# Performance work log

Measured on AMD Instinct MI355X. Metric: run time of the kernel, lower is better.

## Reference

```python
import jax, jax.numpy as jnp
import numpy as np

D = 1024; DI = 2048; HS = 16; PS = DI // HS; NS = 64; KC = 4; CHUNK = 64
HA = 16; HKV = 4; PA = D // HA; MLP_MULT = 4; ROPE_BASE = 10000.0
B_SZ = 2; L_SEQ = 2048


def rms_norm(x):
    eps = jnp.asarray(jnp.finfo(x.dtype).eps, x.dtype)
    return x * jax.lax.rsqrt(jnp.mean(jnp.square(x), axis=-1, keepdims=True) + eps)


def silu(x):
    return x * jax.nn.sigmoid(x)


def apply_rope(x, cos, sin):
    half = x.shape[-1] // 2
    x1, x2 = x[..., :half], x[..., half:]
    return jnp.concatenate([x1 * cos + x2 * sin, -x1 * sin + x2 * cos], axis=-1)


def selective_scan(x, A, Bm, Cm, dt, chunk):
    # x: [B,L,H,P], Bm/Cm: [B,L,H,N], A/dt: [H]. L must be a multiple of chunk.
    Bb, L, H, P = x.shape
    N = Bm.shape[-1]
    decay = jnp.exp(A * dt)  # [H]
    nc = L // chunk
    xp = x.reshape(Bb, nc, chunk, H, P).transpose(0, 1, 3, 2, 4)   # [B,nc,H,cs,P]
    Bp = Bm.reshape(Bb, nc, chunk, H, N).transpose(0, 1, 3, 2, 4)  # [B,nc,H,cs,N]
    Cp = Cm.reshape(Bb, nc, chunk, H, N).transpose(0, 1, 3, 2, 4)
    x_dt = xp * dt[None, None, :, None, None]
    idx = jnp.arange(chunk)
    diff = idx[:, None] - idx[None, :]
    # intra-chunk causal decay matrix L_mat: [H,cs,cs]
    Lm = jnp.where(diff >= 0, decay[:, None, None] ** jnp.maximum(diff, 0), 0.0)
    CB = jnp.einsum('bchqn,bchkn->bchqk', Cp, Bp)
    y_diag = jnp.einsum('bchqk,bchkp->bchqp', CB * Lm[None, None], x_dt)
    # per-chunk states
    decay_rev = decay[:, None] ** (chunk - 1 - idx)[None, :]  # [H,cs]
    states = jnp.einsum('bchtn,bchtp->bchnp', Bp * decay_rev[None, None, :, :, None], x_dt)
    # inter-chunk propagation
    ci = jnp.arange(nc)
    shift = ci[:, None] - ci[None, :] - 1
    cdec = decay ** chunk
    M = jnp.where(shift >= 0, cdec[:, None, None] ** jnp.maximum(shift, 0), 0.0)  # [H,nc,nc]
    h_carry = jnp.einsum('hij,bjhnp->bihnp', M, states)
    decay_out = decay[:, None] ** (idx + 1)[None, :]  # [H,cs]
    y_off = jnp.einsum('bchtn,bchnp->bchtp', Cp, h_carry) * decay_out[None, None, :, :, None]
    y = (y_diag + y_off).transpose(0, 1, 3, 2, 4).reshape(Bb, L, H, P)
    return y


def mlp(n, fc_w, proj_w):
    h = jax.nn.relu(n @ fc_w)
    return jnp.square(h) @ proj_w


def setup_inputs() -> dict:
    key = jax.random.key(0)
    ks = jax.random.split(key, 24)
    w = lambda k, shp, s=0.02: jax.random.normal(k, shp, jnp.float32) * s
    dt_init = jax.random.uniform(ks[0], (HS,), jnp.float32, 0.001, 0.1)
    dt_bias = dt_init + jnp.log(-jnp.expm1(-dt_init))  # inverse softplus
    return {
        'x': jax.random.normal(ks[1], (B_SZ, L_SEQ, D), jnp.float32),
        'in_proj_w': w(ks[2], (D, 2 * DI)),
        'conv_w': w(ks[3], (DI, KC), 0.2),
        'conv_b': jnp.zeros((DI,), jnp.float32),
        'B_proj_w': w(ks[4], (D, HS * NS)),
        'C_proj_w': w(ks[5], (D, HS * NS)),
        'dt_bias': dt_bias,
        'A_log': jnp.log(jnp.arange(1, HS + 1, dtype=jnp.float32)),
        'D_param': jnp.ones((HS,), jnp.float32),
        'out_proj_w': w(ks[6], (DI, D)),
        'resid_mix_m': jnp.stack([jnp.ones(D), jnp.zeros(D)]).astype(jnp.float32),
        'mamba_scale': jnp.ones((D,), jnp.float32),
        'm_fc_w': w(ks[7], (D, MLP_MULT * D)),
        'm_proj_w': w(ks[8], (MLP_MULT * D, D)),
        'm_mlp_scale': jnp.ones((D,), jnp.float32),
        'resid_mix_a': jnp.stack([jnp.ones(D), jnp.zeros(D)]).astype(jnp.float32),
        'q_w': w(ks[9], (D, D)),
        'k_w': w(ks[10], (D, HKV * PA)),
        'v_w': w(ks[11], (D, HKV * PA)),
        'o_w': w(ks[12], (D, D)),
        'q_gain': jnp.full((HA,), 1.0, jnp.float32),
        'attn_scale': jnp.ones((D,), jnp.float32),
        'a_fc_w': w(ks[13], (D, MLP_MULT * D)),
        'a_proj_w': w(ks[14], (MLP_MULT * D, D)),
        'a_mlp_scale': jnp.ones((D,), jnp.float32),
    }


def reference(x, in_proj_w, conv_w, conv_b, B_proj_w, C_proj_w, dt_bias, A_log, D_param, out_proj_w, resid_mix_m, mamba_scale, m_fc_w, m_proj_w, m_mlp_scale, resid_mix_a, q_w, k_w, v_w, o_w, q_gain, attn_scale, a_fc_w, a_proj_w, a_mlp_scale):
    Bb, L, _ = x.shape
    x0 = x
    # ---- Mamba block ----
    xm = resid_mix_m[0][None, None] * x + resid_mix_m[1][None, None] * x0
    n = rms_norm(xm)
    vg = n @ in_proj_w
    value, gate = vg[..., :DI], vg[..., DI:]
    v_t = value.transpose(0, 2, 1)  # [B, DI, L]
    v_conv = jax.lax.conv_general_dilated(
        v_t, conv_w[:, None, :], (1,), [(KC - 1, 0)],
        feature_group_count=DI, dimension_numbers=('NCH', 'OIH', 'NCH')) + conv_b[None, :, None]
    value = silu(v_conv).transpose(0, 2, 1).reshape(Bb, L, HS, PS)
    Bm = (xm @ B_proj_w).reshape(Bb, L, HS, NS)  # B/C use pre-norm (mixed) input
    Cm = (xm @ C_proj_w).reshape(Bb, L, HS, NS)
    dt = jax.nn.softplus(dt_bias)
    A = -jnp.exp(A_log)
    y = selective_scan(value, A, Bm, Cm, dt, CHUNK)
    y = y + D_param[None, None, :, None] * value
    y = (y.reshape(Bb, L, DI) * silu(gate)) @ out_proj_w
    xm = xm + mamba_scale[None, None] * y
    xm = xm + m_mlp_scale[None, None] * mlp(rms_norm(xm), m_fc_w, m_proj_w)
    # ---- Attention block ----
    xa = resid_mix_a[0][None, None] * xm + resid_mix_a[1][None, None] * x0
    n = rms_norm(xa)
    q = (n @ q_w).reshape(Bb, L, HA, PA).transpose(0, 2, 1, 3)
    k = (n @ k_w).reshape(Bb, L, HKV, PA).transpose(0, 2, 1, 3)
    v = (n @ v_w).reshape(Bb, L, HKV, PA).transpose(0, 2, 1, 3)
    q = rms_norm(q); k = rms_norm(k)
    inv_freq = 1.0 / (ROPE_BASE ** (jnp.arange(0, PA, 2, dtype=jnp.float32) / PA))
    f = jnp.outer(jnp.arange(L, dtype=jnp.float32), inv_freq)
    cos, sin = jnp.cos(f)[None, None], jnp.sin(f)[None, None]
    q = apply_rope(q, cos, sin) * q_gain[None, :, None, None]
    k = apply_rope(k, cos, sin)
    G = HA // HKV
    k = jnp.repeat(k, G, axis=1); v = jnp.repeat(v, G, axis=1)
    s = jnp.einsum('bhqd,bhkd->bhqk', q, k) / np.float32(np.sqrt(PA))
    mask = jnp.tril(jnp.ones((L, L), bool))
    s = jnp.where(mask[None, None], s, jnp.asarray(-jnp.inf, s.dtype))
    att = jax.nn.softmax(s, axis=-1)
    y = jnp.einsum('bhqk,bhkd->bhqd', att, v).transpose(0, 2, 1, 3).reshape(Bb, L, D)
    xa = xa + attn_scale[None, None] * (y @ o_w)
    xa = xa + a_mlp_scale[None, None] * mlp(rms_norm(xa), a_fc_w, a_proj_w)
    return xa
```

## Files before the change

kernel.cpp:

```cpp
#include <hip/hip_runtime.h>
#include <hip/hip_bf16.h>
#include <math.h>

#define D_ 1024
#define DI_ 2048
#define HS_ 16
#define PS_ 128
#define NS_ 64
#define HA_ 16
#define HKV_ 4
#define PA_ 64
#define B_ 2
#define L_ 2048
#define NT_ 4096
#define NC_ 32
#define RMS_EPS_ 1.1920929e-7f

typedef __attribute__((ext_vector_type(8))) short short8;
typedef __attribute__((ext_vector_type(4))) float f32x4;

#define GLOAD_LDS16(gp, lp)                                                        \
  __builtin_amdgcn_global_load_lds(                                               \
      (const __attribute__((address_space(1))) unsigned int*)(gp),                \
      (__attribute__((address_space(3))) unsigned int*)(lp), 16, 0, 0)

__global__ __launch_bounds__(256) void transpose_cvt(
    const float* __restrict__ W, __hip_bfloat16* __restrict__ Wt, int K, int N, int ldw) {
  __shared__ float t[32][33];
  int n0 = blockIdx.x * 32, k0 = blockIdx.y * 32;
  int tx = threadIdx.x & 31, ty = threadIdx.x >> 5;
#pragma unroll
  for (int i = 0; i < 4; i++)
    t[ty + i * 8][tx] = W[(size_t)(k0 + ty + i * 8) * ldw + n0 + tx];
  __syncthreads();
#pragma unroll
  for (int i = 0; i < 4; i++)
    Wt[(size_t)(n0 + ty + i * 8) * K + k0 + tx] = __float2bfloat16(t[tx][ty + i * 8]);
}

template<int MODE>
__global__ __launch_bounds__(512) void gemm256_k32(
    const unsigned short* __restrict__ A, const unsigned short* __restrict__ Wt,
    __hip_bfloat16* __restrict__ Cb, int N, int K) {
  __shared__ unsigned short As[3][256 * 32];
  __shared__ unsigned short Bs[3][256 * 32];
  int lid = blockIdx.x;
  int x = lid & 7, r = lid >> 3;
  int bm = ((x >> 2) * 8 + (r & 7)) * 256;
  int bn = ((x & 3) * 4 + (r >> 3)) * 256;
  int tid = threadIdx.x;
  int w = tid >> 6, l = tid & 63;
  int wr = w >> 2, wc = w & 3;
  int l15 = l & 15, lg = l >> 4;
  int rr = tid >> 2, ss = tid & 3;

  f32x4 acc[8][4];
#pragma unroll
  for (int i = 0; i < 8; i++)
#pragma unroll
    for (int j = 0; j < 4; j++) acc[i][j] = (f32x4){0.f, 0.f, 0.f, 0.f};

  auto STAGE = [&](int kt, int nb) {
    int k0 = kt * 32;
#pragma unroll
    for (int p = 0; p < 2; p++) {
      int row = p * 128 + rr;
      int kq = ss ^ ((row >> 1) & 3);
      GLOAD_LDS16(A + (size_t)(bm + row) * K + k0 + kq * 8, &As[nb][row * 32 + ss * 8]);
    }
#pragma unroll
    for (int p = 0; p < 2; p++) {
      int row = p * 128 + rr;
      int kq = ss ^ ((row >> 1) & 3);
      GLOAD_LDS16(Wt + (size_t)(bn + row) * K + k0 + kq * 8, &Bs[nb][row * 32 + ss * 8]);
    }
  };

  int KT = K >> 5;
  STAGE(0, 0);
  STAGE(1, 1);
  int buf = 0;
  for (int t = 0; t < KT; ++t) {
    if (t + 1 < KT) {
      asm volatile("s_waitcnt vmcnt(4)" ::: "memory");
    } else {
      asm volatile("s_waitcnt vmcnt(0)" ::: "memory");
    }
    __builtin_amdgcn_s_barrier();
    __builtin_amdgcn_sched_barrier(0);
    if (t + 2 < KT) STAGE(t + 2, (t + 2) % 3);
    short8 bf[4];
#pragma unroll
    for (int j = 0; j < 4; j++) {
      int row = wc * 64 + j * 16 + l15;
      bf[j] = *(const short8*)&Bs[buf][row * 32 + ((lg ^ ((row >> 1) & 3)) << 3)];
    }
#pragma unroll
    for (int i = 0; i < 8; i++) {
      int row = wr * 128 + i * 16 + l15;
      short8 af = *(const short8*)&As[buf][row * 32 + ((lg ^ ((row >> 1) & 3)) << 3)];
#pragma unroll
      for (int j = 0; j < 4; j++)
        acc[i][j] = __builtin_amdgcn_mfma_f32_16x16x32_bf16(af, bf[j], acc[i][j], 0, 0, 0);
    }
    buf = (buf == 2) ? 0 : buf + 1;
  }
#pragma unroll
  for (int i = 0; i < 8; i++)
#pragma unroll
    for (int j = 0; j < 4; j++) {
      int gr = bm + wr * 128 + i * 16 + lg * 4;
      int gc = bn + wc * 64 + j * 16 + l15;
#pragma unroll
      for (int reg = 0; reg < 4; reg++) {
        float v = acc[i][j][reg];
        if (MODE == 1) { v = fmaxf(v, 0.f); v = v * v; }
        Cb[(size_t)(gr + reg) * N + gc] = __float2bfloat16(v);
      }
    }
}
// ... 23 lines not shown
  int tid = threadIdx.x;
  int w = tid >> 6, l = tid & 63;
  int wr = w / nWc, wc = w % nWc;
  int l15 = l & 15, lg = l >> 4;
  f32x4 acc[MF][4];
#pragma unroll
  for (int i = 0; i < MF; i++)
#pragma unroll
    for (int j = 0; j < 4; j++) acc[i][j] = (f32x4){0.f, 0.f, 0.f, 0.f};
  int r_ = tid >> 3;
  int s_ = tid & 7;

  auto STAGE = [&](int k0, int nb) {
#pragma unroll
    for (int i = 0; i < 4; i++) {
      int rr = i * 32 + r_;
      int kq = s_ ^ (rr & 7);
      GLOAD_LDS16(A + (size_t)(bm + rr) * K + k0 + kq * 8, &As[nb][rr * 64 + s_ * 8]);
    }
#pragma unroll
    for (int i = 0; i < BN / 32; i++) {
      int rr = i * 32 + r_;
      int kq = s_ ^ (rr & 7);
      GLOAD_LDS16(Wt + (size_t)(bn + rr) * K + k0 + kq * 8, &Bs[nb][rr * 64 + s_ * 8]);
    }
  };

  STAGE(0, 0);
  __syncthreads();
  int cur = 0;
  for (int k0 = 0; k0 < K; k0 += 64) {
    if (k0 + 64 < K) STAGE(k0 + 64, cur ^ 1);
#pragma unroll
    for (int h = 0; h < 2; h++) {
      short8 af[MF], bfr[4];
#pragma unroll
      for (int i = 0; i < MF; i++) {
        int row = wr * (16 * MF) + i * 16 + l15;
        int c = h * 4 + lg;
        af[i] = *(const short8*)&As[cur][row * 64 + ((c ^ (row & 7)) << 3)];
      }
#pragma unroll
      for (int j = 0; j < 4; j++) {
        int row = wc * 64 + j * 16 + l15;
        int c = h * 4 + lg;
        bfr[j] = *(const short8*)&Bs[cur][row * 64 + ((c ^ (row & 7)) << 3)];
      }
#pragma unroll
      for (int i = 0; i < MF; i++)
#pragma unroll
        for (int j = 0; j < 4; j++)
          acc[i][j] = __builtin_amdgcn_mfma_f32_16x16x32_bf16(af[i], bfr[j], acc[i][j], 0, 0, 0);
    }
    __syncthreads();
    cur ^= 1;
  }
  int rb = lg * 4, cb2 = l15;
#pragma unroll
  for (int i = 0; i < MF; i++)
#pragma unroll
    for (int j = 0; j < 4; j++) {
      int gr = bm + wr * (16 * MF) + i * 16 + rb;
      int gc = bn + wc * 64 + j * 16 + cb2;
#pragma unroll
      for (int reg = 0; reg < 4; reg++) {
        float v = acc[i][j][reg];
        size_t idx = (size_t)(gr + reg) * N + gc;
        if (mode == 0) {
          Cf[idx] = v;
        } else if (mode == 1) {
          v = fmaxf(v, 0.f);
          Cb[idx] = __float2bfloat16(v * v);
        } else if (mode == 2) {
          Cb[idx] = __float2bfloat16(v);
        } else {
          Cf[idx] = baseb[idx] + scale[gc] * v;
        }
      }
    }
}

__global__ __launch_bounds__(256) void gemm64(
    const unsigned short* __restrict__ A, const unsigned short* __restrict__ Wt,
    float* __restrict__ Cf, const float* __restrict__ baseb,
    const float* __restrict__ scale, int N, int K, int mode) {
  __shared__ unsigned short As[2][64 * 64];
  __shared__ unsigned short Bs[2][64 * 64];
  int lid = blockIdx.x;
  int x = lid & 7, r = lid >> 3;
  int bm = (x * 8 + (r & 7)) * 64;
  int bn = (r >> 3) * 64;
  int tid = threadIdx.x;
  int w = tid >> 6, l = tid & 63;
  int l15 = l & 15, lg = l >> 4;
  f32x4 acc[4];
#pragma unroll
  for (int j = 0; j < 4; j++) acc[j] = (f32x4){0.f, 0.f, 0.f, 0.f};
  int r_ = tid >> 3;
  int s_ = tid & 7;

  auto STAGE = [&](int k0, int nb) {
#pragma unroll
    for (int i = 0; i < 2; i++) {
      int row = i * 32 + r_;
      int kq = s_ ^ (row & 7);
      GLOAD_LDS16(A + (size_t)(bm + row) * K + k0 + kq * 8, &As[nb][row * 64 + s_ * 8]);
    }
#pragma unroll
    for (int i = 0; i < 2; i++) {
      int row = i * 32 + r_;
      int kq = s_ ^ (row & 7);
      GLOAD_LDS16(Wt + (size_t)(bn + row) * K + k0 + kq * 8, &Bs[nb][row * 64 + s_ * 8]);
    }
  };

  STAGE(0, 0);
  __syncthreads();
  int cur = 0;
  for (int k0 = 0; k0 < K; k0 += 64) {
    if (k0 + 64 < K) STAGE(k0 + 64, cur ^ 1);
#pragma unroll
    for (int h = 0; h < 2; h++) {
      int c = h * 4 + lg;
      int arow = w * 16 + l15;
      short8 af = *(const short8*)&As[cur][arow * 64 + ((c ^ (arow & 7)) << 3)];
#pragma unroll
      for (int j = 0; j < 4; j++) {
        int brow = j * 16 + l15;
        short8 bfr = *(const short8*)&Bs[cur][brow * 64 + ((c ^ (brow & 7)) << 3)];
        acc[j] = __builtin_amdgcn_mfma_f32_16x16x32_bf16(af, bfr, acc[j], 0, 0, 0);
      }
    }
    __syncthreads();
    cur ^= 1;
  }
#pragma unroll
  for (int j = 0; j < 4; j++) {
    int gr = bm + w * 16 + lg * 4;
    int gc = bn + j * 16 + l15;
#pragma unroll
    for (int reg = 0; reg < 4; reg++) {
      float v = acc[j][reg];
      size_t idx = (size_t)(gr + reg) * N + gc;
      if (mode == 0) Cf[idx] = v;
      else           Cf[idx] = baseb[idx] + scale[gc] * v;
    }
  }
}

__global__ __launch_bounds__(256) void mix_rms_kernel(
    const float* __restrict__ a, const float* __restrict__ b2,
    const float* __restrict__ mix, float* __restrict__ xout,
    __hip_bfloat16* __restrict__ nbf, __hip_bfloat16* __restrict__ rawbf) {
  int row = blockIdx.x;
  size_t base = (size_t)row * D_;
  float v[4]; float ss = 0.f;
#pragma unroll
  for (int i = 0; i < 4; i++) {
    int d = threadIdx.x + i * 256;
    float val = mix[d] * a[base + d] + mix[D_ + d] * b2[base + d];
    v[i] = val; ss += val * val;
  }
  for (int o = 32; o > 0; o >>= 1) ss += __shfl_down(ss, o, 64);
  __shared__ float red[4];
  if ((threadIdx.x & 63) == 0) red[threadIdx.x >> 6] = ss;
  __syncthreads();
  float inv = rsqrtf((red[0] + red[1] + red[2] + red[3]) * (1.f / D_) + RMS_EPS_);
#pragma unroll
  for (int i = 0; i < 4; i++) {
    int d = threadIdx.x + i * 256;
    xout[base + d] = v[i];
    nbf[base + d] = __float2bfloat16(v[i] * inv);
    if (rawbf) rawbf[base + d] = __float2bfloat16(v[i]);
  }
}

__global__ __launch_bounds__(256) void rms_kernel(
    const float* __restrict__ a, __hip_bfloat16* __restrict__ nbf) {
  int row = blockIdx.x;
  size_t base = (size_t)row * D_;
  float v[4]; float ss = 0.f;
#pragma unroll
  for (int i = 0; i < 4; i++) {
    int d = threadIdx.x + i * 256;
    float val = a[base + d];
    v[i] = val; ss += val * val;
  }
  for (int o = 32; o > 0; o >>= 1) ss += __shfl_down(ss, o, 64);
  __shared__ float red[4];
  if ((threadIdx.x & 63) == 0) red[threadIdx.x >> 6] = ss;
  __syncthreads();
  float inv = rsqrtf((red[0] + red[1] + red[2] + red[3]) * (1.f / D_) + RMS_EPS_);
#pragma unroll
  for (int i = 0; i < 4; i++) {
    int d = threadIdx.x + i * 256;
    nbf[base + d] = __float2bfloat16(v[i] * inv);
  }
}

__global__ __launch_bounds__(256) void conv_silu_kernel(
    const __hip_bfloat16* __restrict__ vg, const float* __restrict__ cw,
    const float* __restrict__ cb, float* __restrict__ xv) {
  int idx = blockIdx.x * 256 + threadIdx.x;
  int c = idx & (DI_ - 1);
  int bl = idx >> 11;
  int l = bl & (L_ - 1);
  float acc = cb[c];
  float w0 = cw[c * 4 + 0], w1 = cw[c * 4 + 1], w2 = cw[c * 4 + 2], w3 = cw[c * 4 + 3];
  size_t rb = (size_t)bl * 4096 + c;
  if (l >= 3) acc += __bfloat162float(vg[rb - (size_t)3 * 4096]) * w0;
  if (l >= 2) acc += __bfloat162float(vg[rb - (size_t)2 * 4096]) * w1;
  if (l >= 1) acc += __bfloat162float(vg[rb - (size_t)1 * 4096]) * w2;
  acc += __bfloat162float(vg[rb]) * w3;
  xv[idx] = acc / (1.f + __expf(-acc));
}

__global__ __launch_bounds__(256) void scanA1_kernel(
    const float* __restrict__ xv, const __hip_bfloat16* __restrict__ BCm,
    const float* __restrict__ dt_bias, const float* __restrict__ A_log,
    float* __restrict__ st) {
  __shared__ __align__(16) float sm[4096 + 8192];
  float* Bs = sm;
  float* Xs = sm + 4096;
  int blk = blockIdx.x;
  int c = blk & 31, h = (blk >> 5) & 15, b = blk >> 9;
  float dt = log1pf(__expf(dt_bias[h]));
  float adt = -__expf(A_log[h]) * dt;
  int tid = threadIdx.x;
  int l0 = c * 64;
  size_t rB = ((size_t)(b * L_ + l0)) * 2048 + h * NS_;
#pragma unroll
  for (int i = 0; i < 16; i++) {
    int e = tid + i * 256;
    int t = e >> 6, n = e & 63;
    Bs[t * 64 + n] = __bfloat162float(BCm[rB + (size_t)t * 2048 + n]);
  }
  size_t rX = ((size_t)(b * L_ + l0)) * DI_ + h * PS_;
#pragma unroll
  for (int i = 0; i < 32; i++) {
    int e = tid + i * 256;
    int t = e >> 7, p = e & 127;
    Xs[t * 128 + p] = xv[rX + (size_t)t * DI_ + p];
  }
  __syncthreads();
  int pg = tid & 31;
  int ng = (tid >> 5) << 3;
  float acc[8][4];
#pragma unroll
  for (int nn = 0; nn < 8; nn++)
#pragma unroll
    for (int i = 0; i < 4; i++) acc[nn][i] = 0.f;
  for (int t = 0; t < 64; t++) {
    float dr = __expf(adt * (float)(63 - t));
    float4 x4 = *(const float4*)&Xs[t * 128 + pg * 4];
    float xd0 = x4.x * dr, xd1 = x4.y * dr, xd2 = x4.z * dr, xd3 = x4.w * dr;
#pragma unroll
    for (int nn = 0; nn < 8; nn++) {
      float bv = Bs[t * 64 + ng + nn];
      acc[nn][0] += bv * xd0; acc[nn][1] += bv * xd1;
      acc[nn][2] += bv * xd2; acc[nn][3] += bv * xd3;
    }
  }
  size_t sb = ((size_t)((b * HS_ + h) * NC_ + c)) * (NS_ * PS_);
#pragma unroll
  for (int nn = 0; nn < 8; nn++) {
    *(float4*)&st[sb + (size_t)(ng + nn) * PS_ + pg * 4] =
        make_float4(acc[nn][0] * dt, acc[nn][1] * dt, acc[nn][2] * dt, acc[nn][3] * dt);
  }
}

__global__ __launch_bounds__(256) void scanA2_kernel(
    const float* __restrict__ xv, const __hip_bfloat16* __restrict__ BCm,
    const float* __restrict__ dt_bias,
    const float* __restrict__ A_log, const float* __restrict__ D_param,
    float* __restrict__ y) {
  __shared__ __align__(16) float sm[4160 + 8192];
  float* Cb = sm;
  float* Bs = sm + 4160;
  float* Xs = sm + 4160;
  int blk = blockIdx.x;
  int c = blk & 31, h = (blk >> 5) & 15, b = blk >> 9;
  float dt = log1pf(__expf(dt_bias[h]));
  float adt = -__expf(A_log[h]) * dt;
  float Dp = D_param[h];
  int tid = threadIdx.x;
  int l0 = c * 64;
  size_t rB = ((size_t)(b * L_ + l0)) * 2048 + h * NS_;
#pragma unroll
  for (int i = 0; i < 16; i++) {
    int e = tid + i * 256;
    int t = e >> 6, n = e & 63;
    Bs[t * 64 + n] = __bfloat162float(BCm[rB + (size_t)t * 2048 + n]);
    Cb[t * 65 + n] = __bfloat162float(BCm[rB + 1024 + (size_t)t * 2048 + n]);
  }
  __syncthreads();
  int q = tid >> 2;
  int kb = (tid & 3) << 4;
  float cbl[16];
#pragma unroll
  for (int kk = 0; kk < 16; kk++) {
    int k = kb + kk;
    float a = 0.f;
    if (k <= q) {
      for (int n = 0; n < 64; n++) a += Cb[q * 65 + n] * Bs[k * 64 + n];
      a *= __expf(adt * (float)(q - k));
    }
    cbl[kk] = a;
  }
  __syncthreads();
#pragma unroll
  for (int kk = 0; kk < 16; kk++) Cb[q * 65 + kb + kk] = cbl[kk];
  size_t rX = ((size_t)(b * L_ + l0)) * DI_ + h * PS_;
#pragma unroll
  for (int i = 0; i < 32; i++) {
    int e = tid + i * 256;
    int t = e >> 7, p = e & 127;
    Xs[t * 128 + p] = xv[rX + (size_t)t * DI_ + p];
  }
  __syncthreads();
  int pg = tid & 31;
  int qg = (tid >> 5) << 3;
  float acc[8][4];
#pragma unroll
  for (int qq = 0; qq < 8; qq++)
#pragma unroll
    for (int i = 0; i < 4; i++) acc[qq][i] = 0.f;
  for (int k = 0; k < 64; k++) {
    float4 x4 = *(const float4*)&Xs[k * 128 + pg * 4];
#pragma unroll
    for (int qq = 0; qq < 8; qq++) {
      float s = Cb[(qg + qq) * 65 + k];
      acc[qq][0] += s * x4.x; acc[qq][1] += s * x4.y;
      acc[qq][2] += s * x4.z; acc[qq][3] += s * x4.w;
    }
  }
#pragma unroll
  for (int qq = 0; qq < 8; qq++) {
    int qr = qg + qq;
    float4 xq = *(const float4*)&Xs[qr * 128 + pg * 4];
    size_t yo = ((size_t)(b * L_ + l0 + qr)) * DI_ + h * PS_ + pg * 4;
    *(float4*)&y[yo] = make_float4(acc[qq][0] * dt + Dp * xq.x,
                                   acc[qq][1] * dt + Dp * xq.y,
                                   acc[qq][2] * dt + Dp * xq.z,
                                   acc[qq][3] * dt + Dp * xq.w);
  }
}

__global__ __launch_bounds__(256) void scanB1_kernel(
    float* __restrict__ st, const float* __restrict__ dt_bias,
    const float* __restrict__ A_log) {
  int slice = blockIdx.x & 3;
  int h = (blockIdx.x >> 2) & 15, b = blockIdx.x >> 6;
  float dt = log1pf(__expf(dt_bias[h]));
  float adt = -__expf(A_log[h]) * dt;
  float cdec = __expf(adt * 64.f);
  size_t base = ((size_t)(b * HS_ + h)) * NC_ * (NS_ * PS_) + slice * 2048 + threadIdx.x;
  float hreg[8];
#pragma unroll
  for (int j = 0; j < 8; j++) hreg[j] = 0.f;
  for (int c = 0; c < NC_; c++) {
    size_t o = base + (size_t)c * (NS_ * PS_);
#pragma unroll
    for (int j = 0; j < 8; j++) {
      float tmp = st[o + (size_t)j * 256];
      st[o + (size_t)j * 256] = hreg[j];
      hreg[j] = cdec * hreg[j] + tmp;
    }
  }
}

__global__ __launch_bounds__(256) void scanB2_kernel(
    const __hip_bfloat16* __restrict__ BCm, const float* __restrict__ st,
    const __hip_bfloat16* __restrict__ vg, const float* __restrict__ dt_bias,
    const float* __restrict__ A_log, const float* __restrict__ y,
    __hip_bfloat16* __restrict__ yout) {
  __shared__ float Cs[64 * 64];
  __shared__ __align__(16) float Hs[64 * 128];
  int blk = blockIdx.x;
  int c = blk & 31, h = (blk >> 5) & 15, b = blk >> 9;
  float dt = log1pf(__expf(dt_bias[h]));
  float adt = -__expf(A_log[h]) * dt;
  int tid = threadIdx.x;
  int l0 = c * 64;
  size_t rC = ((size_t)(b * L_ + l0)) * 2048 + 1024 + h * NS_;
#pragma unroll
  for (int i = 0; i < 16; i++) {
    int e = tid + i * 256;
    int t = e >> 6, n = e & 63;
    Cs[t * 64 + n] = __bfloat162float(BCm[rC + (size_t)t * 2048 + n]);
  }
  size_t sb = ((size_t)((b * HS_ + h) * NC_ + c)) * (NS_ * PS_);
#pragma unroll
  for (int i = 0; i < 32; i++) {
    int e = tid + i * 256;
    Hs[e] = st[sb + e];
  }
  __syncthreads();
  int pg = tid & 31;
  int tg = (tid >> 5) << 3;
  float acc[8][4];
#pragma unroll
  for (int tt = 0; tt < 8; tt++)
#pragma unroll
    for (int i = 0; i < 4; i++) acc[tt][i] = 0.f;
  for (int n = 0; n < 64; n++) {
    float4 h4 = *(const float4*)&Hs[n * 128 + pg * 4];
#pragma unroll
    for (int tt = 0; tt < 8; tt++) {
      float cv = Cs[(tg + tt) * 64 + n];
      acc[tt][0] += cv * h4.x; acc[tt][1] += cv * h4.y;
      acc[tt][2] += cv * h4.z; acc[tt][3] += cv * h4.w;
    }
  }
#pragma unroll
  for (int tt = 0; tt < 8; tt++) {
    int t = tg + tt;
    float dout = __expf(adt * (float)(t + 1));
    size_t row = (size_t)(b * L_ + l0 + t);
#pragma unroll
    for (int i = 0; i < 4; i++) {
      int p = pg * 4 + i;
      float g = __bfloat162float(vg[row * 4096 + 2048 + h * PS_ + p]);
      float yv = y[row * DI_ + h * PS_ + p] + acc[tt][i] * dout;
      yout[row * DI_ + h * PS_ + p] = __float2bfloat16(yv * (g / (1.f + __expf(-g))));
    }
  }
}

__global__ void rope_fill_kernel(float* __restrict__ cosb, float* __restrict__ sinb) {
  int idx = blockIdx.x * 256 + threadIdx.x;
  int i = idx & 31, l = idx >> 5;
  float inv = __expf(-(2.0f * (float)i / (float)PA_) * logf(10000.0f));
  float ang = (float)l * inv;
  cosb[idx] = cosf(ang);
  sinb[idx] = sinf(ang);
}

__global__ __launch_bounds__(256) void qknorm_rope_bf16_kernel(
    const float* __restrict__ src, int srcstride, int srcofs,
    __hip_bfloat16* __restrict__ dst, int nh,
    const float* __restrict__ cosb, const float* __restrict__ sinb,
    const float* __restrict__ gain) {
  int row = blockIdx.x * 4 + (threadIdx.x >> 6);
  int lane = threadIdx.x & 63;
  int h = row % nh;
  int tok = row / nh;
  int l = tok & (L_ - 1);
  float v = src[(size_t)tok * srcstride + srcofs + h * 64 + lane];
  float ss = v * v;
  for (int o = 32; o > 0; o >>= 1) ss += __shfl_xor(ss, o, 64);
  v *= rsqrtf(ss * (1.f / PA_) + RMS_EPS_);
  float partner = __shfl_xor(v, 32, 64);
  int i = lane & 31;
  float cth = cosb[l * 32 + i], sth = sinb[l * 32 + i];
  float out = (lane < 32) ? (v * cth + partner * sth) : (v * cth - partner * sth);
  if (gain) out *= gain[h];
  dst[(size_t)tok * (nh * 64) + h * 64 + lane] = __float2bfloat16(out);
}

__global__ __launch_bounds__(256) void attn_mfma_kernel(
    const unsigned short* __restrict__ qb, const unsigned short* __restrict__ kb,
    const unsigned short* __restrict__ vt, const float* __restrict__ qgain,
    __hip_bfloat16* __restrict__ ao) {
  __shared__ unsigned short Ks[64][72];
  __shared__ unsigned short Vs[64][72];
  __shared__ unsigned short Psm[4][16][72];
  int blk = blockIdx.x;
  int qi = blk & 15;
  int h  = (blk >> 4) & 15;
  int b  = blk >> 8;
  int hk = h >> 2;
  int tid = threadIdx.x;
  int w = tid >> 6, l = tid & 63;
  int l15 = l & 15, lg = l >> 4;
  int r0 = tid >> 3, s0 = tid & 7;
  float mstat = 8.0f * fabsf(qgain[h]);
  const unsigned short* kbase = kb + (size_t)b * L_ * (HKV_ * PA_) + hk * PA_ + s0 * 8;
  const unsigned short* vbase = vt + ((size_t)(b * HKV_ + hk) * PA_) * L_ + s0 * 8;

  for (int pass = 0; pass < 2; pass++) {
    int qt = pass ? (31 - qi) : qi;
    int q0 = qt * 64;
    int qw = q0 + w * 16;
    short8 qf[2];
    {
      size_t qrow = ((size_t)(b * L_ + qw + l15)) * (HA_ * PA_) + h * PA_;
      qf[0] = *(const short8*)&qb[qrow + lg * 8];
      qf[1] = *(const short8*)&qb[qrow + 32 + lg * 8];
    }
    f32x4 o_acc[4];
#pragma unroll
    for (int db = 0; db < 4; db++) o_acc[db] = (f32x4){0.f, 0.f, 0.f, 0.f};
    f32x4 lsum = (f32x4){0.f, 0.f, 0.f, 0.f};
    int nkt = qt + 1;
    short8 kr0 = *(const short8*)&kbase[(size_t)r0 * (HKV_ * PA_)];
    short8 kr1 = *(const short8*)&kbase[(size_t)(r0 + 32) * (HKV_ * PA_)];
    short8 vr0 = *(const short8*)&vbase[(size_t)r0 * L_];
    short8 vr1 = *(const short8*)&vbase[(size_t)(r0 + 32) * L_];
    for (int kt = 0; kt < nkt; kt++) {
      int k0 = kt * 64;
      __syncthreads();
      *(short8*)&Ks[r0][s0 * 8] = kr0;
      *(short8*)&Ks[r0 + 32][s0 * 8] = kr1;
      *(short8*)&Vs[r0][s0 * 8] = vr0;
      *(short8*)&Vs[r0 + 32][s0 * 8] = vr1;
      if (kt + 1 < nkt) {
        int k1 = k0 + 64;
        kr0 = *(const short8*)&kbase[(size_t)(k1 + r0) * (HKV_ * PA_)];
        kr1 = *(const short8*)&kbase[(size_t)(k1 + r0 + 32) * (HKV_ * PA_)];
        vr0 = *(const short8*)&vbase[(size_t)r0 * L_ + k1];
        vr1 = *(const short8*)&vbase[(size_t)(r0 + 32) * L_ + k1];
      }
      __syncthreads();
      f32x4 s_acc[4];
#pragma unroll
      for (int kb2 = 0; kb2 < 4; kb2++) {
        short8 b0 = *(const short8*)&Ks[kb2 * 16 + l15][lg * 8];
        short8 b1 = *(const short8*)&Ks[kb2 * 16 + l15][32 + lg * 8];
        f32x4 s = (f32x4){0.f, 0.f, 0.f, 0.f};
        s = __builtin_amdgcn_mfma_f32_16x16x32_bf16(qf[0], b0, s, 0, 0, 0);
        s = __builtin_amdgcn_mfma_f32_16x16x32_bf16(qf[1], b1, s, 0, 0, 0);
        s_acc[kb2] = s;
      }
      bool diag = (kt == qt);
#pragma unroll
      for (int kb2 = 0; kb2 < 4; kb2++) {
        int key = k0 + kb2 * 16 + l15;
#pragma unroll
        for (int reg = 0; reg < 4; reg++) {
          float p = __expf(s_acc[kb2][reg] * 0.125f - mstat);
          if (diag && key > qw + lg * 4 + reg) p = 0.f;
          lsum[reg] += p;
          __hip_bfloat16 hv = __float2bfloat16(p);
          Psm[w][lg * 4 + reg][kb2 * 16 + l15] = *(unsigned short*)&hv;
        }
      }
      asm volatile("s_waitcnt lgkmcnt(0)" ::: "memory");
#pragma unroll
      for (int ks = 0; ks < 2; ks++) {
        short8 pa = *(const short8*)&Psm[w][l15][ks * 32 + lg * 8];
#pragma unroll
        for (int db = 0; db < 4; db++) {
          short8 vb8 = *(const short8*)&Vs[db * 16 + l15][ks * 32 + lg * 8];
          o_acc[db] = __builtin_amdgcn_mfma_f32_16x16x32_bf16(pa, vb8, o_acc[db], 0, 0, 0);
        }
      }
    }
#pragma unroll
    for (int of = 1; of < 16; of <<= 1) {
      lsum[0] += __shfl_xor(lsum[0], of, 64);
      lsum[1] += __shfl_xor(lsum[1], of, 64);
      lsum[2] += __shfl_xor(lsum[2], of, 64);
      lsum[3] += __shfl_xor(lsum[3], of, 64);
    }
#pragma unroll
    for (int reg = 0; reg < 4; reg++) {
      float invl = 1.0f / lsum[reg];
      size_t row = (size_t)(b * L_ + qw + lg * 4 + reg);
#pragma unroll
      for (int db = 0; db < 4; db++)
        ao[row * D_ + h * PA_ + db * 16 + l15] = __float2bfloat16(o_acc[db][reg] * invl);
    }
  }
}

extern "C" void kernel_launch(void* const* d_in, const int* in_sizes, int n_in,
                              void* d_out, int out_size, void* d_ws, size_t ws_size,
                              hipStream_t stream) {
  (void)in_sizes; (void)n_in; (void)out_size; (void)ws_size;
  const float* x           = (const float*)d_in[0];
  const float* in_proj_w   = (const float*)d_in[1];
  const float* conv_w      = (const float*)d_in[2];
  const float* conv_b      = (const float*)d_in[3];
  const float* B_proj_w    = (const float*)d_in[4];
  const float* C_proj_w    = (const float*)d_in[5];
  const float* dt_bias     = (const float*)d_in[6];
  const float* A_log       = (const float*)d_in[7];
  const float* D_param     = (const float*)d_in[8];
  const float* out_proj_w  = (const float*)d_in[9];
  const float* resid_mix_m = (const float*)d_in[10];
  const float* mamba_scale = (const float*)d_in[11];
  const float* m_fc_w      = (const float*)d_in[12];
  const float* m_proj_w    = (const float*)d_in[13];
  const float* m_mlp_scale = (const float*)d_in[14];
  const float* resid_mix_a = (const float*)d_in[15];
  const float* q_w         = (const float*)d_in[16];
  const float* k_w         = (const float*)d_in[17];
  const float* v_w         = (const float*)d_in[18];
  const float* o_w         = (const float*)d_in[19];
  const float* q_gain      = (const float*)d_in[20];
  const float* attn_scale  = (const float*)d_in[21];
  const float* a_fc_w      = (const float*)d_in[22];
  const float* a_proj_w    = (const float*)d_in[23];
  const float* a_mlp_scale = (const float*)d_in[24];
  float* ws  = (float*)d_ws;
  float* out = (float*)d_out;

  float* xm    = ws;
  float* vgR   = ws + 4194304;
  float* xvR   = ws + 12582912;
  float* stR   = ws + 20971520;
  float* nbR   = ws + 29360128;
  float* xmbR  = ws + 31457280;
  float* BCR   = ws + 33554432;
  float* WtR   = ws + 37748736;
  float* cosb  = ws + 51642368;
  float* sinb  = cosb + 65536;

  __hip_bfloat16* vg  = (__hip_bfloat16*)vgR;
  float*          qkvf = vgR;
  float*          xv  = xvR;
  float*          st  = stR;
  __hip_bfloat16* hb  = (__hip_bfloat16*)stR;
  __hip_bfloat16* nbb = (__hip_bfloat16*)nbR;
  __hip_bfloat16* xmb = (__hip_bfloat16*)xmbR;
  __hip_bfloat16* ybb = (__hip_bfloat16*)nbR;
  __hip_bfloat16* BCm = (__hip_bfloat16*)BCR;
  __hip_bfloat16* qbb = (__hip_bfloat16*)xvR;
  __hip_bfloat16* kbb = (__hip_bfloat16*)(xvR + 2097152);
  __hip_bfloat16* vtb = (__hip_bfloat16*)(xvR + 2621440);
  __hip_bfloat16* aob = (__hip_bfloat16*)(xvR + 3145728);

  __hip_bfloat16* Wt = (__hip_bfloat16*)WtR;
  size_t o_in  = 0;
  size_t o_B   = o_in  + (size_t)4096 * 1024;
  size_t o_out = o_B   + (size_t)2048 * 1024;
  size_t o_mfc = o_out + (size_t)1024 * 2048;
  size_t o_mpj = o_mfc + (size_t)4096 * 1024;
  size_t o_qkv = o_mpj + (size_t)1024 * 4096;
  size_t o_o   = o_qkv + (size_t)1536 * 1024;
  size_t o_afc = o_o   + (size_t)1024 * 1024;
  size_t o_apj = o_afc + (size_t)4096 * 1024;

#define TCVT(Wp, off, K, N) \
  transpose_cvt<<<dim3((N) / 32, (K) / 32), 256, 0, stream>>>((Wp), Wt + (off), (K), (N), (N))
  TCVT(in_proj_w,  o_in,  1024, 4096);
  TCVT(B_proj_w,   o_B,   1024, 1024);
  TCVT(C_proj_w,   o_B + (size_t)1024 * 1024, 1024, 1024);
  TCVT(out_proj_w, o_out, 2048, 1024);
  TCVT(m_fc_w,     o_mfc, 1024, 4096);
  TCVT(m_proj_w,   o_mpj, 4096, 1024);
  TCVT(q_w,        o_qkv, 1024, 1024);
  TCVT(k_w,        o_qkv + (size_t)1024 * 1024, 1024, 256);
  TCVT(v_w,        o_qkv + (size_t)1280 * 1024, 1024, 256);
  TCVT(o_w,        o_o,   1024, 1024);
  TCVT(a_fc_w,     o_afc, 1024, 4096);
  TCVT(a_proj_w,   o_apj, 4096, 1024);
#undef TCVT

#define GEMM(BN, Abuf, Woff, Cfp, Cbp, basep, scalep, N, K, mode, rsh) \
  gemm_bf16_t<BN><<<32 * ((N) / (BN)), 256, 0, stream>>>( \
      (const unsigned short*)(Abuf), (const unsigned short*)(Wt + (Woff)), \
      (Cfp), (Cbp), (basep), (scalep), (N), (K), (N) / (BN), (mode), (rsh))
#define GEMM64(Abuf, Woff, Cfp, basep, scalep, N, K, mode) \
  gemm64<<<64 * ((N) / 64), 256, 0, stream>>>( \
      (const unsigned short*)(Abuf), (const unsigned short*)(Wt + (Woff)), \
      (Cfp), (basep), (scalep), (N), (K), (mode))
#define GEMM256(MODE, Abuf, Woff, Cbp) \
  gemm256_k32<MODE><<<256, 512, 0, stream>>>( \
      (const unsigned short*)(Abuf), (const unsigned short*)(Wt + (Woff)), \
      (Cbp), 4096, 1024)

  mix_rms_kernel<<<NT_, 256, 0, stream>>>(x, x, resid_mix_m, xm, nbb, xmb);
  GEMM256(2, nbb, o_in, vg);
  GEMM(128, xmb, o_B, (float*)0, BCm, (const float*)0, (const float*)0, 2048, 1024, 2, 0);
  conv_silu_kernel<<<NT_ * DI_ / 256, 256, 0, stream>>>(vg, conv_w, conv_b, xv);
  scanA1_kernel<<<B_ * HS_ * NC_, 256, 0, stream>>>(xv, BCm, dt_bias, A_log, st);
  scanA2_kernel<<<B_ * HS_ * NC_, 256, 0, stream>>>(xv, BCm, dt_bias, A_log, D_param, xv);
  scanB1_kernel<<<B_ * HS_ * 4, 256, 0, stream>>>(st, dt_bias, A_log);
  scanB2_kernel<<<B_ * HS_ * NC_, 256, 0, stream>>>(BCm, st, vg, dt_bias, A_log, xv, ybb);
  GEMM64(ybb, o_out, xm, xm, mamba_scale, 1024, 2048, 3);
  rms_kernel<<<NT_, 256, 0, stream>>>(xm, nbb);
  GEMM256(1, nbb, o_mfc, hb);
  GEMM64(hb, o_mpj, xm, xm, m_mlp_scale, 1024, 4096, 3);
  mix_rms_kernel<<<NT_, 256, 0, stream>>>(xm, x, resid_mix_a, xm, nbb, (__hip_bfloat16*)0);
  GEMM64(nbb, o_qkv, qkvf, (const float*)0, (const float*)0, 1536, 1024, 0);
  rope_fill_kernel<<<L_ * 32 / 256, 256, 0, stream>>>(cosb, sinb);
  qknorm_rope_bf16_kernel<<<NT_ * HA_ / 4, 256, 0, stream>>>(qkvf, 1536, 0, qbb, HA_, cosb, sinb, q_gain);
  qknorm_rope_bf16_kernel<<<NT_ * HKV_ / 4, 256, 0, stream>>>(qkvf, 1536, 1024, kbb, HKV_, cosb, sinb, (const float*)0);
  transpose_cvt<<<dim3(256 / 32, 2048 / 32), 256, 0, stream>>>(qkvf + 1280, vtb, 2048, 256, 1536);
  transpose_cvt<<<dim3(256 / 32, 2048 / 32), 256, 0, stream>>>(qkvf + (size_t)L_ * 1536 + 1280, vtb + (size_t)256 * L_, 2048, 256, 1536);
  attn_mfma_kernel<<<B_ * HA_ * 16, 256, 0, stream>>>(
      (const unsigned short*)qbb, (const unsigned short*)kbb, (const unsigned short*)vtb,
      q_gain, aob);
  GEMM64(aob, o_o, xm, xm, attn_scale, 1024, 1024, 3);
  rms_kernel<<<NT_, 256, 0, stream>>>(xm, nbb);
  GEMM256(1, nbb, o_afc, hb);
  GEMM64(hb, o_apj, out, xm, a_mlp_scale, 1024, 4096, 3);
#undef GEMM
#undef GEMM64
#undef GEMM256
}
```

Measured before the change: 669.9 us.

## Fuse conv+SiLU into chunk scan kernel and emit QKV projection in bf16

Merges the depthwise conv+SiLU, the chunk-state kernel (scanA1) and the intra-chunk output kernel (scanA2) into one kernel. It recomputes the conv from bf16 vg with a 3-row halo in LDS and keeps x in bf16 in shared memory, so the fp32 xv round trip to global memory and two launches go away. Separately, the QKV GEMM now writes bf16 output, and the qk-norm/rope and V transpose kernels read bf16. This halves that traffic but rounds the activations to bf16 earlier, a small precision risk.

```diff
diff --git a/kernel.cpp b/kernel.cpp
--- a/kernel.cpp
+++ b/kernel.cpp
@@ -17,12 +17,19 @@
 #define RMS_EPS_ 1.1920929e-7f
 
 typedef __attribute__((ext_vector_type(8))) short short8;
+typedef __attribute__((ext_vector_type(4))) short short4v;
 typedef __attribute__((ext_vector_type(4))) float f32x4;
 
 #define GLOAD_LDS16(gp, lp)                                                        \
   __builtin_amdgcn_global_load_lds(                                               \
       (const __attribute__((address_space(1))) unsigned int*)(gp),                \
       (__attribute__((address_space(3))) unsigned int*)(lp), 16, 0, 0)
+
+__device__ __forceinline__ float b2f(unsigned short u) {
+  union { unsigned int i; float f; } x;
+  x.i = ((unsigned int)u) << 16;
+  return x.f;
+}
 
 __global__ __launch_bounds__(256) void transpose_cvt(
     const float* __restrict__ W, __hip_bfloat16* __restrict__ Wt, int K, int N, int ldw) {
@@ -36,6 +43,21 @@
 #pragma unroll
   for (int i = 0; i < 4; i++)
     Wt[(size_t)(n0 + ty + i * 8) * K + k0 + tx] = __float2bfloat16(t[tx][ty + i * 8]);
+}
+
+__global__ __launch_bounds__(256) void transpose_bf16(
+    const unsigned short* __restrict__ S, unsigned short* __restrict__ D,
+    int K, int N, int lds) {
+  __shared__ unsigned short t[32][33];
+  int n0 = blockIdx.x * 32, k0 = blockIdx.y * 32;
+  int tx = threadIdx.x & 31, ty = threadIdx.x >> 5;
+#pragma unroll
+  for (int i = 0; i < 4; i++)
+    t[ty + i * 8][tx] = S[(size_t)(k0 + ty + i * 8) * lds + n0 + tx];
+  __syncthreads();
+#pragma unroll
+  for (int i = 0; i < 4; i++)
+    D[(size_t)(n0 + ty + i * 8) * K + k0 + tx] = t[tx][ty + i * 8];
 }
 
 template<int MODE>
@@ -225,8 +247,9 @@
 
 __global__ __launch_bounds__(256) void gemm64(
     const unsigned short* __restrict__ A, const unsigned short* __restrict__ Wt,
-    float* __restrict__ Cf, const float* __restrict__ baseb,
-    const float* __restrict__ scale, int N, int K, int mode) {
+    float* __restrict__ Cf, __hip_bfloat16* __restrict__ Cbo,
+    const float* __restrict__ baseb, const float* __restrict__ scale,
+    int N, int K, int mode) {
   __shared__ unsigned short As[2][64 * 64];
   __shared__ unsigned short Bs[2][64 * 64];
   int lid = blockIdx.x;
@@ -285,8 +308,9 @@
     for (int reg = 0; reg < 4; reg++) {
       float v = acc[j][reg];
       size_t idx = (size_t)(gr + reg) * N + gc;
-      if (mode == 0) Cf[idx] = v;
-      else           Cf[idx] = baseb[idx] + scale[gc] * v;
+      if (mode == 0)      Cf[idx] = v;
+      else if (mode == 2) Cbo[idx] = __float2bfloat16(v);
+      else                Cf[idx] = baseb[idx] + scale[gc] * v;
     }
   }
 }
@@ -341,86 +365,16 @@
   }
 }
 
-__global__ __launch_bounds__(256) void conv_silu_kernel(
-    const __hip_bfloat16* __restrict__ vg, const float* __restrict__ cw,
-    const float* __restrict__ cb, float* __restrict__ xv) {
-  int idx = blockIdx.x * 256 + threadIdx.x;
-  int c = idx & (DI_ - 1);
-  int bl = idx >> 11;
-  int l = bl & (L_ - 1);
-  float acc = cb[c];
-  float w0 = cw[c * 4 + 0], w1 = cw[c * 4 + 1], w2 = cw[c * 4 + 2], w3 = cw[c * 4 + 3];
-  size_t rb = (size_t)bl * 4096 + c;
-  if (l >= 3) acc += __bfloat162float(vg[rb - (size_t)3 * 4096]) * w0;
-  if (l >= 2) acc += __bfloat162float(vg[rb - (size_t)2 * 4096]) * w1;
-  if (l >= 1) acc += __bfloat162float(vg[rb - (size_t)1 * 4096]) * w2;
-  acc += __bfloat162float(vg[rb]) * w3;
-  xv[idx] = acc / (1.f + __expf(-acc));
-}
-
-__global__ __launch_bounds__(256) void scanA1_kernel(
-    const float* __restrict__ xv, const __hip_bfloat16* __restrict__ BCm,
+__global__ __launch_bounds__(256) void scanAF_kernel(
+    const __hip_bfloat16* __restrict__ vg, const __hip_bfloat16* __restrict__ BCm,
+    const float* __restrict__ cw, const float* __restrict__ cbias,
     const float* __restrict__ dt_bias, const float* __restrict__ A_log,
-    float* __restrict__ st) {
-  __shared__ __align__(16) float sm[4096 + 8192];
-  float* Bs = sm;
-  float* Xs = sm + 4096;
-  int blk = blockIdx.x;
-  int c = blk & 31, h = (blk >> 5) & 15, b = blk >> 9;
-  float dt = log1pf(__expf(dt_bias[h]));
-  float adt = -__expf(A_log[h]) * dt;
-  int tid = threadIdx.x;
-  int l0 = c * 64;
-  size_t rB = ((size_t)(b * L_ + l0)) * 2048 + h * NS_;
-#pragma unroll
-  for (int i = 0; i < 16; i++) {
-    int e = tid + i * 256;
-    int t = e >> 6, n = e & 63;
-    Bs[t * 64 + n] = __bfloat162float(BCm[rB + (size_t)t * 2048 + n]);
-  }
-  size_t rX = ((size_t)(b * L_ + l0)) * DI_ + h * PS_;
-#pragma unroll
-  for (int i = 0; i < 32; i++) {
-    int e = tid + i * 256;
-    int t = e >> 7, p = e & 127;
-    Xs[t * 128 + p] = xv[rX + (size_t)t * DI_ + p];
-  }
-  __syncthreads();
-  int pg = tid & 31;
-  int ng = (tid >> 5) << 3;
-  float acc[8][4];
-#pragma unroll
-  for (int nn = 0; nn < 8; nn++)
-#pragma unroll
-    for (int i = 0; i < 4; i++) acc[nn][i] = 0.f;
-  for (int t = 0; t < 64; t++) {
-    float dr = __expf(adt * (float)(63 - t));
-    float4 x4 = *(const float4*)&Xs[t * 128 + pg * 4];
-    float xd0 = x4.x * dr, xd1 = x4.y * dr, xd2 = x4.z * dr, xd3 = x4.w * dr;
-#pragma unroll
-    for (int nn = 0; nn < 8; nn++) {
-      float bv = Bs[t * 64 + ng + nn];
-      acc[nn][0] += bv * xd0; acc[nn][1] += bv * xd1;
-      acc[nn][2] += bv * xd2; acc[nn][3] += bv * xd3;
-    }
-  }
-  size_t sb = ((size_t)((b * HS_ + h) * NC_ + c)) * (NS_ * PS_);
-#pragma unroll
-  for (int nn = 0; nn < 8; nn++) {
-    *(float4*)&st[sb + (size_t)(ng + nn) * PS_ + pg * 4] =
-        make_float4(acc[nn][0] * dt, acc[nn][1] * dt, acc[nn][2] * dt, acc[nn][3] * dt);
-  }
-}
-
-__global__ __launch_bounds__(256) void scanA2_kernel(
-    const float* __restrict__ xv, const __hip_bfloat16* __restrict__ BCm,
-    const float* __restrict__ dt_bias,
-    const float* __restrict__ A_log, const float* __restrict__ D_param,
-    float* __restrict__ y) {
-  __shared__ __align__(16) float sm[4160 + 8192];
-  float* Cb = sm;
-  float* Bs = sm + 4160;
-  float* Xs = sm + 4160;
+    const float* __restrict__ D_param, float* __restrict__ st, float* __restrict__ y) {
+  __shared__ __align__(16) float sm[12544];
+  unsigned short* Xh = (unsigned short*)sm;
+  float* Cb = sm + 4096;
+  float* Bs = sm + 8256;
+  unsigned short* Vg = (unsigned short*)(sm + 8256);
   int blk = blockIdx.x;
   int c = blk & 31, h = (blk >> 5) & 15, b = blk >> 9;
   float dt = log1pf(__expf(dt_bias[h]));
@@ -428,64 +382,122 @@
   float Dp = D_param[h];
   int tid = threadIdx.x;
   int l0 = c * 64;
-  size_t rB = ((size_t)(b * L_ + l0)) * 2048 + h * NS_;
+  size_t rBC = ((size_t)(b * L_ + l0)) * 2048 + h * NS_;
 #pragma unroll
   for (int i = 0; i < 16; i++) {
     int e = tid + i * 256;
     int t = e >> 6, n = e & 63;
-    Bs[t * 64 + n] = __bfloat162float(BCm[rB + (size_t)t * 2048 + n]);
-    Cb[t * 65 + n] = __bfloat162float(BCm[rB + 1024 + (size_t)t * 2048 + n]);
-  }
-  __syncthreads();
-  int q = tid >> 2;
+    Cb[t * 65 + n] = __bfloat162float(BCm[rBC + 1024 + (size_t)t * 2048 + n]);
+  }
+  for (int k = 0; k < 5; k++) {
+    int e = tid + k * 256;
+    if (e < 1072) {
+      int rr = e >> 4, s = e & 15;
+      int gl = l0 - 3 + rr;
+      short8 v;
+      if (gl < 0) v = (short8){0, 0, 0, 0, 0, 0, 0, 0};
+      else v = *(const short8*)((const unsigned short*)vg +
+                ((size_t)(b * L_ + gl)) * 4096 + h * PS_ + s * 8);
+      *(short8*)&Vg[rr * 128 + s * 8] = v;
+    }
+  }
+  __syncthreads();
+  {
+    int p4 = (tid & 31) * 4;
+    int t0 = (tid >> 5) * 8;
+    float w0[4], w1[4], w2[4], w3[4], bb[4];
+#pragma unroll
+    for (int q = 0; q < 4; q++) {
+      int ch = h * PS_ + p4 + q;
+      w0[q] = cw[ch * 4 + 0]; w1[q] = cw[ch * 4 + 1];
+      w2[q] = cw[ch * 4 + 2]; w3[q] = cw[ch * 4 + 3];
+      bb[q] = cbias[ch];
+    }
+#pragma unroll
+    for (int i = 0; i < 8; i++) {
+      int t = t0 + i;
+      short4v r0 = *(const short4v*)&Vg[(t + 0) * 128 + p4];
+      short4v r1 = *(const short4v*)&Vg[(t + 1) * 128 + p4];
+      short4v r2 = *(const short4v*)&Vg[(t + 2) * 128 + p4];
+      short4v r3 = *(const short4v*)&Vg[(t + 3) * 128 + p4];
+      short4v o;
+#pragma unroll
+      for (int q = 0; q < 4; q++) {
+        float a = bb[q] + w0[q] * b2f((unsigned short)r0[q])
+                        + w1[q] * b2f((unsigned short)r1[q])
+                        + w2[q] * b2f((unsigned short)r2[q])
+                        + w3[q] * b2f((unsigned short)r3[q]);
+        float sv = a / (1.f + __expf(-a));
+        __hip_bfloat16 hv = __float2bfloat16(sv);
+        o[q] = *(short*)&hv;
+      }
+      *(short4v*)&Xh[t * 128 + p4] = o;
+    }
+  }
+  __syncthreads();
+#pragma unroll
+  for (int i = 0; i < 16; i++) {
+    int e = tid + i * 256;
+    int t = e >> 6, n = e & 63;
+    Bs[t * 64 + n] = __bfloat162float(BCm[rBC + (size_t)t * 2048 + n]);
+  }
+  __syncthreads();
+  int q_ = tid >> 2;
   int kb = (tid & 3) << 4;
   float cbl[16];
 #pragma unroll
   for (int kk = 0; kk < 16; kk++) {
     int k = kb + kk;
     float a = 0.f;
-    if (k <= q) {
-      for (int n = 0; n < 64; n++) a += Cb[q * 65 + n] * Bs[k * 64 + n];
-      a *= __expf(adt * (float)(q - k));
+    if (k <= q_) {
+      for (int n = 0; n < 64; n++) a += Cb[q_ * 65 + n] * Bs[k * 64 + n];
+      a *= __expf(adt * (float)(q_ - k));
     }
     cbl[kk] = a;
   }
   __syncthreads();
 #pragma unroll
-  for (int kk = 0; kk < 16; kk++) Cb[q * 65 + kb + kk] = cbl[kk];
-  size_t rX = ((size_t)(b * L_ + l0)) * DI_ + h * PS_;
-#pragma unroll
-  for (int i = 0; i < 32; i++) {
-    int e = tid + i * 256;
-    int t = e >> 7, p = e & 127;
-    Xs[t * 128 + p] = xv[rX + (size_t)t * DI_ + p];
-  }
+  for (int kk = 0; kk < 16; kk++) Cb[q_ * 65 + kb + kk] = cbl[kk];
   __syncthreads();
   int pg = tid & 31;
-  int qg = (tid >> 5) << 3;
-  float acc[8][4];
-#pragma unroll
-  for (int qq = 0; qq < 8; qq++)
-#pragma unroll
-    for (int i = 0; i < 4; i++) acc[qq][i] = 0.f;
-  for (int k = 0; k < 64; k++) {
-    float4 x4 = *(const float4*)&Xs[k * 128 + pg * 4];
-#pragma unroll
-    for (int qq = 0; qq < 8; qq++) {
-      float s = Cb[(qg + qq) * 65 + k];
-      acc[qq][0] += s * x4.x; acc[qq][1] += s * x4.y;
-      acc[qq][2] += s * x4.z; acc[qq][3] += s * x4.w;
-    }
+  int ng = (tid >> 5) << 3;
+  float acc1[8][4], acc2[8][4];
+#pragma unroll
+  for (int nn = 0; nn < 8; nn++)
+#pragma unroll
+    for (int i = 0; i < 4; i++) { acc1[nn][i] = 0.f; acc2[nn][i] = 0.f; }
+  for (int t = 0; t < 64; t++) {
+    short4v xr = *(const short4v*)&Xh[t * 128 + pg * 4];
+    float x0 = b2f((unsigned short)xr[0]), x1 = b2f((unsigned short)xr[1]);
+    float x2 = b2f((unsigned short)xr[2]), x3 = b2f((unsigned short)xr[3]);
+    float dr = __expf(adt * (float)(63 - t));
+    float xd0 = x0 * dr, xd1 = x1 * dr, xd2 = x2 * dr, xd3 = x3 * dr;
+#pragma unroll
+    for (int nn = 0; nn < 8; nn++) {
+      float bv = Bs[t * 64 + ng + nn];
+      acc1[nn][0] += bv * xd0; acc1[nn][1] += bv * xd1;
+      acc1[nn][2] += bv * xd2; acc1[nn][3] += bv * xd3;
+      float cv = Cb[(ng + nn) * 65 + t];
+      acc2[nn][0] += cv * x0; acc2[nn][1] += cv * x1;
+      acc2[nn][2] += cv * x2; acc2[nn][3] += cv * x3;
+    }
+  }
+  size_t sb = ((size_t)((b * HS_ + h) * NC_ + c)) * (NS_ * PS_);
+#pragma unroll
+  for (int nn = 0; nn < 8; nn++) {
+    *(float4*)&st[sb + (size_t)(ng + nn) * PS_ + pg * 4] =
+        make_float4(acc1[nn][0] * dt, acc1[nn][1] * dt, acc1[nn][2] * dt, acc1[nn][3] * dt);
   }
 #pragma unroll
   for (int qq = 0; qq < 8; qq++) {
-    int qr = qg + qq;
-    float4 xq = *(const float4*)&Xs[qr * 128 + pg * 4];
+    int qr = ng + qq;
+    short4v xr = *(const short4v*)&Xh[qr * 128 + pg * 4];
     size_t yo = ((size_t)(b * L_ + l0 + qr)) * DI_ + h * PS_ + pg * 4;
-    *(float4*)&y[yo] = make_float4(acc[qq][0] * dt + Dp * xq.x,
-                                   acc[qq][1] * dt + Dp * xq.y,
-                                   acc[qq][2] * dt + Dp * xq.z,
-                                   acc[qq][3] * dt + Dp * xq.w);
+    *(float4*)&y[yo] = make_float4(
+        acc2[qq][0] * dt + Dp * b2f((unsigned short)xr[0]),
+        acc2[qq][1] * dt + Dp * b2f((unsigned short)xr[1]),
+        acc2[qq][2] * dt + Dp * b2f((unsigned short)xr[2]),
+        acc2[qq][3] * dt + Dp * b2f((unsigned short)xr[3]));
   }
 }
 
@@ -580,7 +592,7 @@
 }
 
 __global__ __launch_bounds__(256) void qknorm_rope_bf16_kernel(
-    const float* __restrict__ src, int srcstride, int srcofs,
+    const __hip_bfloat16* __restrict__ src, int srcstride, int srcofs,
     __hip_bfloat16* __restrict__ dst, int nh,
     const float* __restrict__ cosb, const float* __restrict__ sinb,
     const float* __restrict__ gain) {
@@ -589,7 +601,7 @@
   int h = row % nh;
   int tok = row / nh;
   int l = tok & (L_ - 1);
-  float v = src[(size_t)tok * srcstride + srcofs + h * 64 + lane];
+  float v = __bfloat162float(src[(size_t)tok * srcstride + srcofs + h * 64 + lane]);
   float ss = v * v;
   for (int o = 32; o > 0; o >>= 1) ss += __shfl_xor(ss, o, 64);
   v *= rsqrtf(ss * (1.f / PA_) + RMS_EPS_);
@@ -750,19 +762,19 @@
   float* cosb  = ws + 51642368;
   float* sinb  = cosb + 65536;
 
-  __hip_bfloat16* vg  = (__hip_bfloat16*)vgR;
-  float*          qkvf = vgR;
-  float*          xv  = xvR;
-  float*          st  = stR;
-  __hip_bfloat16* hb  = (__hip_bfloat16*)stR;
-  __hip_bfloat16* nbb = (__hip_bfloat16*)nbR;
-  __hip_bfloat16* xmb = (__hip_bfloat16*)xmbR;
-  __hip_bfloat16* ybb = (__hip_bfloat16*)nbR;
-  __hip_bfloat16* BCm = (__hip_bfloat16*)BCR;
-  __hip_bfloat16* qbb = (__hip_bfloat16*)xvR;
-  __hip_bfloat16* kbb = (__hip_bfloat16*)(xvR + 2097152);
-  __hip_bfloat16* vtb = (__hip_bfloat16*)(xvR + 2621440);
-  __hip_bfloat16* aob = (__hip_bfloat16*)(xvR + 3145728);
+  __hip_bfloat16* vg   = (__hip_bfloat16*)vgR;
+  __hip_bfloat16* qkvb = (__hip_bfloat16*)vgR;
+  float*          yv   = xvR;
+  float*          st   = stR;
+  __hip_bfloat16* hb   = (__hip_bfloat16*)stR;
+  __hip_bfloat16* nbb  = (__hip_bfloat16*)nbR;
+  __hip_bfloat16* xmb  = (__hip_bfloat16*)xmbR;
+  __hip_bfloat16* ybb  = (__hip_bfloat16*)nbR;
+  __hip_bfloat16* BCm  = (__hip_bfloat16*)BCR;
+  __hip_bfloat16* qbb  = (__hip_bfloat16*)xvR;
+  __hip_bfloat16* kbb  = (__hip_bfloat16*)(xvR + 2097152);
+  __hip_bfloat16* vtb  = (__hip_bfloat16*)(xvR + 2621440);
+  __hip_bfloat16* aob  = (__hip_bfloat16*)(xvR + 3145728);
 
   __hip_bfloat16* Wt = (__hip_bfloat16*)WtR;
   size_t o_in  = 0;
@@ -795,10 +807,10 @@
   gemm_bf16_t<BN><<<32 * ((N) / (BN)), 256, 0, stream>>>( \
       (const unsigned short*)(Abuf), (const unsigned short*)(Wt + (Woff)), \
       (Cfp), (Cbp), (basep), (scalep), (N), (K), (N) / (BN), (mode), (rsh))
-#define GEMM64(Abuf, Woff, Cfp, basep, scalep, N, K, mode) \
+#define GEMM64(Abuf, Woff, Cfp, Cbop, basep, scalep, N, K, mode) \
   gemm64<<<64 * ((N) / 64), 256, 0, stream>>>( \
       (const unsigned short*)(Abuf), (const unsigned short*)(Wt + (Woff)), \
-      (Cfp), (basep), (scalep), (N), (K), (mode))
+      (Cfp), (Cbop), (basep), (scalep), (N), (K), (mode))
 #define GEMM256(MODE, Abuf, Woff, Cbp) \
   gemm256_k32<MODE><<<256, 512, 0, stream>>>( \
       (const unsigned short*)(Abuf), (const unsigned short*)(Wt + (Woff)), \
@@ -807,29 +819,31 @@
   mix_rms_kernel<<<NT_, 256, 0, stream>>>(x, x, resid_mix_m, xm, nbb, xmb);
   GEMM256(2, nbb, o_in, vg);
   GEMM(128, xmb, o_B, (float*)0, BCm, (const float*)0, (const float*)0, 2048, 1024, 2, 0);
-  conv_silu_kernel<<<NT_ * DI_ / 256, 256, 0, stream>>>(vg, conv_w, conv_b, xv);
-  scanA1_kernel<<<B_ * HS_ * NC_, 256, 0, stream>>>(xv, BCm, dt_bias, A_log, st);
-  scanA2_kernel<<<B_ * HS_ * NC_, 256, 0, stream>>>(xv, BCm, dt_bias, A_log, D_param, xv);
+  scanAF_kernel<<<B_ * HS_ * NC_, 256, 0, stream>>>(vg, BCm, conv_w, conv_b,
+                                                    dt_bias, A_log, D_param, st, yv);
   scanB1_kernel<<<B_ * HS_ * 4, 256, 0, stream>>>(st, dt_bias, A_log);
-  scanB2_kernel<<<B_ * HS_ * NC_, 256, 0, stream>>>(BCm, st, vg, dt_bias, A_log, xv, ybb);
-  GEMM64(ybb, o_out, xm, xm, mamba_scale, 1024, 2048, 3);
+  scanB2_kernel<<<B_ * HS_ * NC_, 256, 0, stream>>>(BCm, st, vg, dt_bias, A_log, yv, ybb);
+  GEMM64(ybb, o_out, xm, (__hip_bfloat16*)0, xm, mamba_scale, 1024, 2048, 3);
   rms_kernel<<<NT_, 256, 0, stream>>>(xm, nbb);
   GEMM256(1, nbb, o_mfc, hb);
-  GEMM64(hb, o_mpj, xm, xm, m_mlp_scale, 1024, 4096, 3);
+  GEMM64(hb, o_mpj, xm, (__hip_bfloat16*)0, xm, m_mlp_scale, 1024, 4096, 3);
   mix_rms_kernel<<<NT_, 256, 0, stream>>>(xm, x, resid_mix_a, xm, nbb, (__hip_bfloat16*)0);
-  GEMM64(nbb, o_qkv, qkvf, (const float*)0, (const float*)0, 1536, 1024, 0);
+  GEMM64(nbb, o_qkv, (float*)0, qkvb, (const float*)0, (const float*)0, 1536, 1024, 2);
   rope_fill_kernel<<<L_ * 32 / 256, 256, 0, stream>>>(cosb, sinb);
-  qknorm_rope_bf16_kernel<<<NT_ * HA_ / 4, 256, 0, stream>>>(qkvf, 1536, 0, qbb, HA_, cosb, sinb, q_gain);
-  qknorm_rope_bf16_kernel<<<NT_ * HKV_ / 4, 256, 0, stream>>>(qkvf, 1536, 1024, kbb, HKV_, cosb, sinb, (const float*)0);
-  transpose_cvt<<<dim3(256 / 32, 2048 / 32), 256, 0, stream>>>(qkvf + 1280, vtb, 2048, 256, 1536);
-  transpose_cvt<<<dim3(256 / 32, 2048 / 32), 256, 0, stream>>>(qkvf + (size_t)L_ * 1536 + 1280, vtb + (size_t)256 * L_, 2048, 256, 1536);
+  qknorm_rope_bf16_kernel<<<NT_ * HA_ / 4, 256, 0, stream>>>(qkvb, 1536, 0, qbb, HA_, cosb, sinb, q_gain);
+  qknorm_rope_bf16_kernel<<<NT_ * HKV_ / 4, 256, 0, stream>>>(qkvb, 1536, 1024, kbb, HKV_, cosb, sinb, (const float*)0);
+  transpose_bf16<<<dim3(256 / 32, 2048 / 32), 256, 0, stream>>>(
+      (const unsigned short*)qkvb + 1280, (unsigned short*)vtb, 2048, 256, 1536);
+  transpose_bf16<<<dim3(256 / 32, 2048 / 32), 256, 0, stream>>>(
+      (const unsigned short*)qkvb + (size_t)L_ * 1536 + 1280,
+      (unsigned short*)vtb + (size_t)256 * L_, 2048, 256, 1536);
   attn_mfma_kernel<<<B_ * HA_ * 16, 256, 0, stream>>>(
       (const unsigned short*)qbb, (const unsigned short*)kbb, (const unsigned short*)vtb,
       q_gain, aob);
-  GEMM64(aob, o_o, xm, xm, attn_scale, 1024, 1024, 3);
+  GEMM64(aob, o_o, xm, (__hip_bfloat16*)0, xm, attn_scale, 1024, 1024, 3);
   rms_kernel<<<NT_, 256, 0, stream>>>(xm, nbb);
   GEMM256(1, nbb, o_afc, hb);
-  GEMM64(hb, o_apj, out, xm, a_mlp_scale, 1024, 4096, 3);
+  GEMM64(hb, o_apj, out, (__hip_bfloat16*)0, xm, a_mlp_scale, 1024, 4096, 3);
 #undef GEMM
 #undef GEMM64
 #undef GEMM256
```

After: 636.7 us. 1.05x faster.
